# Performance work log

Hardware: AMD Instinct MI355X
Metric: run time of the kernel (lower is better)

The kernel has to match this reference:

```python
import jax, jax.numpy as jnp
import numpy as np

L, B, T, D, F = 2, 128, 512, 64, 512  # num_layers, batch, seq_len, input_dim, n_features


def setup_inputs() -> dict:
    key = jax.random.key(0)
    ks = jax.random.split(key, 16)
    s = 1.0 / np.sqrt(F)
    u = lambda k, shape: jax.random.uniform(k, shape, jnp.float32, -s, s)
    return {
        "x": jax.random.normal(ks[0], (L, B, D), jnp.float32),
        "last_feat": jax.random.normal(ks[1], (B, F), jnp.float32),
        "W_init": u(ks[2], (F, D)), "b_init": u(ks[3], (F,)),
        "W_ih0": u(ks[4], (4 * F, F)), "W_hh0": u(ks[5], (4 * F, F)),
        "b_ih0": u(ks[6], (4 * F,)), "b_hh0": u(ks[7], (4 * F,)),
        "W_ih1": u(ks[8], (4 * F, F)), "W_hh1": u(ks[9], (4 * F, F)),
        "b_ih1": u(ks[10], (4 * F,)), "b_hh1": u(ks[11], (4 * F,)),
        "W_out": u(ks[12], (F, F)), "b_out": u(ks[13], (F,)),
    }


def _lstm_cell(inp, h, c, W_ih, W_hh, b_ih, b_hh):
    # torch gate order: i, f, g, o
    gates = inp @ W_ih.T + b_ih + h @ W_hh.T + b_hh
    i, f, g, o = jnp.split(gates, 4, axis=-1)
    c_new = jax.nn.sigmoid(f) * c + jax.nn.sigmoid(i) * jnp.tanh(g)
    h_new = jax.nn.sigmoid(o) * jnp.tanh(c_new)
    return h_new, c_new


def reference(x, last_feat, W_init, b_init, W_ih0, W_hh0, b_ih0, b_hh0,
              W_ih1, W_hh1, b_ih1, b_hh1, W_out, b_out):
    # hidden and cell are BOTH initial_layer(x) -> identical initial states (L, B, F)
    h0 = x @ W_init.T + b_init
    c0 = h0

    def step(carry, _):
        out, h, c = carry  # out: (B,F); h,c: (L,B,F)
        h0n, c0n = _lstm_cell(out, h[0], c[0], W_ih0, W_hh0, b_ih0, b_hh0)
        h1n, c1n = _lstm_cell(h0n, h[1], c[1], W_ih1, W_hh1, b_ih1, b_hh1)
        # output_layer(out) in the original is computed but discarded (dead code)
        new_carry = (h1n, jnp.stack([h0n, h1n]), jnp.stack([c0n, c1n]))
        return new_carry, h1n

    _, outs = jax.lax.scan(step, (last_feat, h0, c0), None, length=T)  # (T, B, F)
    # faithful to torch: outputs.reshape((batch, seq_len, n_features)) — a raw reshape
    return outs.reshape(B, T, F)
```

## Files before the change

### kernel.cpp

```cpp
#include <hip/hip_runtime.h>
#include <hip/hip_bf16.h>

#define FDIM   512
#define BATCH  128
#define TSTEPS 512
#define GDIM   2048
#define NPH    (2*TSTEPS)

typedef __attribute__((ext_vector_type(8))) short bf16x8;
typedef __attribute__((ext_vector_type(4))) float f32x4;

union AfU { bf16x8 v; unsigned long long q[2]; };

__device__ __forceinline__ ushort f32_to_bf16(float v) {
    union { float f; unsigned u; } c; c.f = v;
    unsigned b = c.u;
    return (ushort)((b + 0x7FFFu + ((b >> 16) & 1u)) >> 16);
}
__device__ __forceinline__ float fsigmoid(float x) {
    return __fdividef(1.0f, 1.0f + __expf(-x));
}
__device__ __forceinline__ float ftanh(float x) {
    return 1.0f - __fdividef(2.0f, __expf(2.0f * x) + 1.0f);
}

__device__ __forceinline__ unsigned long long aload64(const unsigned long long* p) {
    return __hip_atomic_load(p, __ATOMIC_RELAXED, __HIP_MEMORY_SCOPE_AGENT);
}
__device__ __forceinline__ unsigned aload32(const unsigned* p) {
    return __hip_atomic_load(p, __ATOMIC_RELAXED, __HIP_MEMORY_SCOPE_AGENT);
}
__device__ __forceinline__ void astore32(unsigned* p, unsigned v) {
    __hip_atomic_store(p, v, __ATOMIC_RELAXED, __HIP_MEMORY_SCOPE_AGENT);
}

__global__ __launch_bounds__(256) void convert_weights(
    const float* __restrict__ Wih0, const float* __restrict__ Whh0,
    const float* __restrict__ Wih1, const float* __restrict__ Whh1,
    const float* __restrict__ bih0, const float* __restrict__ bhh0,
    const float* __restrict__ bih1, const float* __restrict__ bhh1,
    ushort* __restrict__ wcat, float* __restrict__ bc)
{
    int idx = blockIdx.x * 256 + threadIdx.x;
    if (idx < 2 * GDIM * 1024) {
        int kk = idx & 1023;
        int r  = (idx >> 10) & 2047;
        int L  = idx >> 21;
        const float* Wih = L ? Wih1 : Wih0;
        const float* Whh = L ? Whh1 : Whh0;
        float v = (kk < 512) ? Wih[(size_t)r * 512 + kk] : Whh[(size_t)r * 512 + (kk - 512)];
        wcat[idx] = f32_to_bf16(v);
    }
    if (idx < 2 * GDIM) {
        int L = idx >> 11, r = idx & 2047;
        bc[idx] = L ? (bih1[r] + bhh1[r]) : (bih0[r] + bhh0[r]);
    }
}

__global__ __launch_bounds__(512, 2) void lstm_persistent(
    const float* __restrict__ x,
    const float* __restrict__ Winit,
    const float* __restrict__ binit,
    const float* __restrict__ lastf,
    const ushort* __restrict__ wcat,
    const float* __restrict__ bc,
    ushort* __restrict__ hst,
    ushort* __restrict__ lfbuf,
    unsigned* __restrict__ flags,
    float* __restrict__ out)
{
    const int tid  = threadIdx.x;
    const int lane = tid & 63;
    const int wave = tid >> 6;
    const int myL  = wave >> 2;
    const int kq   = wave & 3;
    const int g    = blockIdx.x & 7;
    const int ft   = blockIdx.x >> 3;
    const int wgid = g * 32 + ft;

    const int r16 = (tid >> 4) & 15;
    const int cc  = tid & 15;
    const int myB = g * 16 + r16;
    const int myF = ft * 16 + cc;

    __shared__ float part[4][4][16][16];

    float c_reg;
    {
        const float* xr = x + ((size_t)myL * BATCH + myB) * 64;
        const float* wr = Winit + (size_t)myF * 64;
        float s = binit[myF];
        #pragma unroll
        for (int k = 0; k < 64; ++k) s += xr[k] * wr[k];
        c_reg = s;
        unsigned hv = f32_to_bf16(s);
        unsigned up = (unsigned)__shfl_xor((int)hv, 1);
        if (!(cc & 1))
            astore32((unsigned*)(hst + (((size_t)myL * 2 + 1) * BATCH + myB) * FDIM + myF),
                     hv | (up << 16));
    }
    if (myL == 0) {
        float v = lastf[(size_t)myB * FDIM + myF];
        unsigned hv = f32_to_bf16(v);
        unsigned up = (unsigned)__shfl_xor((int)hv, 1);
        if (!(cc & 1))
            astore32((unsigned*)(lfbuf + (size_t)myB * FDIM + myF), hv | (up << 16));
    }
    float bias[4];
    #pragma unroll
    for (int ct = 0; ct < 4; ++ct) bias[ct] = bc[myL * GDIM + ct * FDIM + myF];

    bf16x8 bw[4][8];
    {
        const int wl = lane & 15, kg0 = lane >> 4;
        #pragma unroll
        for (int ct = 0; ct < 4; ++ct) {
            const ushort* base = wcat + ((size_t)myL * GDIM + ct * FDIM + ft * 16 + wl) * 1024
                               + kq * 256 + kg0 * 8;
            #pragma unroll
            for (int ks = 0; ks < 8; ++ks)
                bw[ct][ks] = *reinterpret_cast<const bf16x8*>(base + ks * 32);
        }
    }
    #pragma unroll
    for (int ct = 0; ct < 4; ++ct)
        #pragma unroll
        for (int ks = 0; ks < 8; ++ks)
            asm volatile("" : "+v"(bw[ct][ks]));

    __syncthreads();
    if (tid == 0) astore32(&flags[wgid], 1u);

    const int rA = lane & 15, kg = lane >> 4;

    for (int ph = 0; ph < NPH; ++ph) {
        const int L = ph & 1;
        const int t = ph >> 1;
        const bool active = (myL == L);

        const ushort* srcInp = (L == 0)
            ? (t == 0 ? lfbuf : hst + (size_t)(2 + ((t - 1) & 1)) * BATCH * FDIM)
            : (hst + (size_t)(t & 1) * BATCH * FDIM);
        const ushort* srcOwn = hst + (size_t)(L * 2 + ((t - 1) & 1)) * BATCH * FDIM;
        const ushort* arow = ((kq < 2) ? srcInp : srcOwn)
                           + (size_t)(g * 16 + rA) * FDIM + (kq & 1) * 256 + kg * 8;

        bf16x8 af[8];
        const bool pre = active && (kq >= 2) && (ph > 0);
        if (pre) {
            #pragma unroll
            for (int ks = 0; ks < 8; ++ks) {
                AfU u;
                u.q[0] = aload64((const unsigned long long*)(arow + ks * 32));
                u.q[1] = aload64((const unsigned long long*)(arow + ks * 32) + 1);
                af[ks] = u.v;
            }
        }

        if (wave == 0) {
            const unsigned tgt = (unsigned)(ph + 1);
            for (;;) {
                unsigned v = (lane < 32) ? aload32(&flags[g * 32 + lane]) : tgt;
                if (__all((int)(v >= tgt))) break;
            }
        }
        __syncthreads();

        if (active) {
            if (!pre) {
                #pragma unroll
                for (int ks = 0; ks < 8; ++ks) {
                    AfU u;
                    u.q[0] = aload64((const unsigned long long*)(arow + ks * 32));
                    u.q[1] = aload64((const unsigned long long*)(arow + ks * 32) + 1);
                    af[ks] = u.v;
                }
            }
            f32x4 acc[4] = {{0,0,0,0},{0,0,0,0},{0,0,0,0},{0,0,0,0}};
            #pragma unroll
            for (int ks = 0; ks < 8; ++ks) {
                #pragma unroll
                for (int ct = 0; ct < 4; ++ct)
                    acc[ct] = __builtin_amdgcn_mfma_f32_16x16x32_bf16(af[ks], bw[ct][ks], acc[ct], 0, 0, 0);
            }
            const int n = lane & 15, q = lane >> 4;
            #pragma unroll
            for (int ct = 0; ct < 4; ++ct)
                #pragma unroll
                for (int j = 0; j < 4; ++j)
                    part[kq][ct][q * 4 + j][n] = acc[ct][j];
        }
        __syncthreads();

        float hn = 0.0f;
        if (active) {
            float gate[4];
            #pragma unroll
            for (int ct = 0; ct < 4; ++ct)
                gate[ct] = bias[ct] + part[0][ct][r16][cc] + part[1][ct][r16][cc]
                         + part[2][ct][r16][cc] + part[3][ct][r16][cc];
            float ig = fsigmoid(gate[0]);
            float fg = fsigmoid(gate[1]);
            float gg = ftanh(gate[2]);
            float og = fsigmoid(gate[3]);
            float cn = fg * c_reg + ig * gg;
            hn = og * ftanh(cn);
            c_reg = cn;
            unsigned hv = f32_to_bf16(hn);
            unsigned up = (unsigned)__shfl_xor((int)hv, 1);
            if (!(cc & 1))
                astore32((unsigned*)(hst + ((size_t)(L * 2 + (t & 1)) * BATCH + myB) * FDIM + myF),
                         hv | (up << 16));
        }
        __syncthreads();
        if (tid == 0) astore32(&flags[wgid], (unsigned)(ph + 2));
        if (active && L == 1) out[((size_t)t * BATCH + myB) * FDIM + myF] = hn;
    }
}

extern "C" void kernel_launch(void* const* d_in, const int* in_sizes, int n_in,
                              void* d_out, int out_size, void* d_ws, size_t ws_size,
                              hipStream_t stream)
{
    const float* x      = (const float*)d_in[0];
    const float* lastf  = (const float*)d_in[1];
    const float* W_init = (const float*)d_in[2];
    const float* b_init = (const float*)d_in[3];
    const float* W_ih0  = (const float*)d_in[4];
    const float* W_hh0  = (const float*)d_in[5];
    const float* b_ih0  = (const float*)d_in[6];
    const float* b_hh0  = (const float*)d_in[7];
    const float* W_ih1  = (const float*)d_in[8];
    const float* W_hh1  = (const float*)d_in[9];
    const float* b_ih1  = (const float*)d_in[10];
    const float* b_hh1  = (const float*)d_in[11];
    float* out = (float*)d_out;

    char* ws = (char*)d_ws;
    size_t off = 0;
    ushort*   wcat  = (ushort*)(ws + off);   off += (size_t)2 * GDIM * 1024 * 2;
    float*    bcb   = (float*)(ws + off);    off += (size_t)2 * GDIM * 4;
    ushort*   hstb  = (ushort*)(ws + off);   off += (size_t)2 * 2 * BATCH * FDIM * 2;
    ushort*   lfb   = (ushort*)(ws + off);   off += (size_t)BATCH * FDIM * 2;
    unsigned* flags = (unsigned*)(ws + off); off += 256 * 4;

    hipMemsetAsync(flags, 0, 256 * 4, stream);

    convert_weights<<<(2 * GDIM * 1024 + 255) / 256, 256, 0, stream>>>(
        W_ih0, W_hh0, W_ih1, W_hh1, b_ih0, b_hh0, b_ih1, b_hh1, wcat, bcb);

    lstm_persistent<<<256, 512, 0, stream>>>(
        x, W_init, b_init, lastf, wcat, bcb, hstb, lfb, flags, out);
}
```

Measured before the change: 3.350 ms.

## Use per-wave flags and only wait on the producing layer's flags

Replaces the per-workgroup flag, which was set after a trailing __syncthreads, with a flag per wave per layer. Each wave publishes its flag right after its own h stores drain, via an explicit vmcnt wait, so the end-of-phase block barrier goes away. The poller in each phase now reads only the 128 flags of the layer that produced the previous phase's data, instead of the 32 workgroup flags. The risks are the correctness of the memory ordering without a block barrier, since LDS reuse of part across phases now relies on the next phase's syncthreads, and more flag loads per poll.

```diff
diff --git a/kernel.cpp b/kernel.cpp
--- a/kernel.cpp
+++ b/kernel.cpp
@@ -6,6 +6,7 @@
 #define TSTEPS 512
 #define GDIM   2048
 #define NPH    (2*TSTEPS)
+#define SLOTSZ (BATCH*FDIM)
 
 typedef __attribute__((ext_vector_type(8))) short bf16x8;
 typedef __attribute__((ext_vector_type(4))) float f32x4;
@@ -76,12 +77,13 @@
     const int kq   = wave & 3;
     const int g    = blockIdx.x & 7;
     const int ft   = blockIdx.x >> 3;
-    const int wgid = g * 32 + ft;
 
     const int r16 = (tid >> 4) & 15;
     const int cc  = tid & 15;
     const int myB = g * 16 + r16;
     const int myF = ft * 16 + cc;
+
+    unsigned* const myflag = &flags[((g * 2 + myL) * 32 + ft) * 4 + kq];
 
     __shared__ float part[4][4][16][16];
 
@@ -128,8 +130,8 @@
         for (int ks = 0; ks < 8; ++ks)
             asm volatile("" : "+v"(bw[ct][ks]));
 
-    __syncthreads();
-    if (tid == 0) astore32(&flags[wgid], 1u);
+    asm volatile("s_waitcnt vmcnt(0)" ::: "memory");
+    if (lane == 0) astore32(myflag, 1u);
 
     const int rA = lane & 15, kg = lane >> 4;
 
@@ -139,9 +141,9 @@
         const bool active = (myL == L);
 
         const ushort* srcInp = (L == 0)
-            ? (t == 0 ? lfbuf : hst + (size_t)(2 + ((t - 1) & 1)) * BATCH * FDIM)
-            : (hst + (size_t)(t & 1) * BATCH * FDIM);
-        const ushort* srcOwn = hst + (size_t)(L * 2 + ((t - 1) & 1)) * BATCH * FDIM;
+            ? (t == 0 ? lfbuf : hst + (size_t)(2 + ((t - 1) & 1)) * SLOTSZ)
+            : (hst + (size_t)(t & 1) * SLOTSZ);
+        const ushort* srcOwn = hst + (size_t)(L * 2 + ((t - 1) & 1)) * SLOTSZ;
         const ushort* arow = ((kq < 2) ? srcInp : srcOwn)
                            + (size_t)(g * 16 + rA) * FDIM + (kq & 1) * 256 + kg * 8;
 
@@ -159,9 +161,17 @@
 
         if (wave == 0) {
             const unsigned tgt = (unsigned)(ph + 1);
+            const unsigned* fb = flags + g * 256 + ((ph == 0) ? 0 : (((ph - 1) & 1) << 7));
             for (;;) {
-                unsigned v = (lane < 32) ? aload32(&flags[g * 32 + lane]) : tgt;
-                if (__all((int)(v >= tgt))) break;
+                unsigned a = aload32(fb + lane);
+                unsigned b = aload32(fb + 64 + lane);
+                bool ok = (a >= tgt) && (b >= tgt);
+                if (ph == 0) {
+                    unsigned c2 = aload32(fb + 128 + lane);
+                    unsigned d2 = aload32(fb + 192 + lane);
+                    ok = ok && (c2 >= tgt) && (d2 >= tgt);
+                }
+                if (__all((int)ok)) break;
             }
         }
         __syncthreads();
@@ -192,7 +202,6 @@
         }
         __syncthreads();
 
-        float hn = 0.0f;
         if (active) {
             float gate[4];
             #pragma unroll
@@ -204,17 +213,17 @@
             float gg = ftanh(gate[2]);
             float og = fsigmoid(gate[3]);
             float cn = fg * c_reg + ig * gg;
-            hn = og * ftanh(cn);
+            float hn = og * ftanh(cn);
             c_reg = cn;
             unsigned hv = f32_to_bf16(hn);
             unsigned up = (unsigned)__shfl_xor((int)hv, 1);
             if (!(cc & 1))
                 astore32((unsigned*)(hst + ((size_t)(L * 2 + (t & 1)) * BATCH + myB) * FDIM + myF),
                          hv | (up << 16));
-        }
-        __syncthreads();
-        if (tid == 0) astore32(&flags[wgid], (unsigned)(ph + 2));
-        if (active && L == 1) out[((size_t)t * BATCH + myB) * FDIM + myF] = hn;
+            asm volatile("s_waitcnt vmcnt(0)" ::: "memory");
+            if (lane == 0) astore32(myflag, (unsigned)(ph + 2));
+            if (L == 1) out[((size_t)t * BATCH + myB) * FDIM + myF] = hn;
+        }
     }
 }
 
@@ -242,9 +251,9 @@
     float*    bcb   = (float*)(ws + off);    off += (size_t)2 * GDIM * 4;
     ushort*   hstb  = (ushort*)(ws + off);   off += (size_t)2 * 2 * BATCH * FDIM * 2;
     ushort*   lfb   = (ushort*)(ws + off);   off += (size_t)BATCH * FDIM * 2;
-    unsigned* flags = (unsigned*)(ws + off); off += 256 * 4;
-
-    hipMemsetAsync(flags, 0, 256 * 4, stream);
+    unsigned* flags = (unsigned*)(ws + off); off += (size_t)8 * 256 * 4;
+
+    hipMemsetAsync(flags, 0, (size_t)8 * 256 * 4, stream);
 
     convert_weights<<<(2 * GDIM * 1024 + 255) / 256, 256, 0, stream>>>(
         W_ih0, W_hh0, W_ih1, W_hh1, b_ih0, b_hh0, b_ih1, b_hh1, wcat, bcb);
```

Measured after the change: 4.708 ms. +40.5%, slower.
